# Performance work log

Hardware: AMD Instinct MI355X
Metric: run time of the kernel (lower is better)

## Reference

```python
import jax, jax.numpy as jnp
import numpy as np

B, S, E, H, NQ, FF = 2, 2048, 768, 12, 8, 3072
DK = E // H
EPS = 1e-5


def _layernorm(x, g, b):
    m = jnp.mean(x, axis=-1, keepdims=True)
    v = jnp.mean((x - m) ** 2, axis=-1, keepdims=True)
    return (x - m) * jax.lax.rsqrt(v + EPS) * g + b


def setup_inputs() -> dict:
    key = jax.random.key(0)
    ks = jax.random.split(key, 12)
    s = 0.02
    return {
        'x': jax.random.normal(ks[0], (B, S, E), dtype=jnp.float32),
        'W_o': jax.random.normal(ks[1], (E, E), dtype=jnp.float32) * s,
        'b_o': jnp.zeros((E,), dtype=jnp.float32),
        'g1': jnp.ones((E,), dtype=jnp.float32),
        'be1': jnp.zeros((E,), dtype=jnp.float32),
        'g2': jnp.ones((E,), dtype=jnp.float32),
        'be2': jnp.zeros((E,), dtype=jnp.float32),
        'ry': jax.random.normal(ks[2], (NQ,), dtype=jnp.float32),
        'W1': jax.random.normal(ks[3], (NQ, FF), dtype=jnp.float32) * s,
        'b1': jnp.zeros((FF,), dtype=jnp.float32),
        'W2': jax.random.normal(ks[4], (FF, E), dtype=jnp.float32) * s,
        'b2': jnp.zeros((E,), dtype=jnp.float32),
    }


def reference(x, W_o, b_o, g1, be1, g2, be2, ry, W1, b1, W2, b2):
    # --- multi-head self-attention (q = k = v = x, no QKV projection) ---
    q = x.reshape(B, S, H, DK).transpose(0, 2, 1, 3)  # [B,H,S,DK]
    scores = jnp.einsum('bhqd,bhkd->bhqk', q, q) / jnp.sqrt(jnp.float32(DK))
    attn = jax.nn.softmax(scores, axis=-1)
    out = jnp.einsum('bhqk,bhkd->bhqd', attn, q)
    out = out.transpose(0, 2, 1, 3).reshape(B, S, E)
    attn_out = out @ W_o + b_o

    x = _layernorm(x + attn_out, g1, be1)

    # --- quantum FFN: per-wire RX(x_i) encode, RY(ry_i), <Z> = cos(x_i)*cos(ry_i) ---
    q_meas = jnp.cos(x[..., :NQ]) * jnp.cos(ry)  # [B,S,NQ]
    ffn_out = jax.nn.relu(q_meas @ W1 + b1) @ W2 + b2

    return _layernorm(x + ffn_out, g2, be2)
```

## Files before the change

### kernel.cpp

```cpp
#include <hip/hip_runtime.h>
#include <hip/hip_bf16.h>

#define B_  2
#define S_  2048
#define E_  768
#define H_  12
#define DK_ 64
#define NQ_ 8
#define FF_ 3072
#define EPS_ 1e-5f

typedef __attribute__((ext_vector_type(8))) short short8;
typedef __attribute__((ext_vector_type(4))) float f32x4;
typedef __hip_bfloat16 bf16;

__device__ __forceinline__ bf16 f2bh(float f) { return __float2bfloat16(f); }
__device__ __forceinline__ short f2b(float f) {
    bf16 h = __float2bfloat16(f);
    return *reinterpret_cast<short*>(&h);
}

__device__ __forceinline__ int swz(int row, int col) {
    return (col & 7) | ((((col >> 3) ^ (row & 7)) & 7) << 3);
}

__device__ __forceinline__ f32x4 mfma16(short8 a, short8 b, f32x4 c) {
    return __builtin_amdgcn_mfma_f32_16x16x32_bf16(a, b, c, 0, 0, 0);
}

__device__ __forceinline__ void gload16(const bf16* g, bf16* l) {
    __builtin_amdgcn_global_load_lds(
        (__attribute__((address_space(1))) void*)g,
        (__attribute__((address_space(3))) void*)l, 16, 0, 0);
}

__global__ __launch_bounds__(256) void prep_xall(const float* __restrict__ x,
                                                 bf16* __restrict__ xb,
                                                 bf16* __restrict__ xT) {
    __shared__ float tile[32][33];
    int e0 = blockIdx.x * 32, s0 = blockIdx.y * 32;
    int tx = threadIdx.x & 31, ty = threadIdx.x >> 5;
    int b = s0 >> 11, sl0 = s0 & 2047;
#pragma unroll
    for (int i = 0; i < 4; i++) {
        int row = ty + i * 8;
        float v = x[(size_t)(s0 + row) * E_ + e0 + tx];
        tile[row][tx] = v;
        xb[(size_t)(s0 + row) * E_ + e0 + tx] = f2bh(v);
    }
    __syncthreads();
#pragma unroll
    for (int i = 0; i < 4; i++) {
        int row = ty + i * 8;
        xT[((size_t)b * E_ + e0 + row) * S_ + sl0 + tx] = f2bh(tile[tx][row]);
    }
}

__global__ __launch_bounds__(256) void prep_cvt(const float* __restrict__ x,
                                                bf16* __restrict__ xb, int n4) {
    int i = blockIdx.x * 256 + threadIdx.x;
    if (i >= n4) return;
    float4 f = *(const float4*)(x + (size_t)i * 4);
    short4 sv;
    sv.x = f2b(f.x); sv.y = f2b(f.y); sv.z = f2b(f.z); sv.w = f2b(f.w);
    *(short4*)((short*)xb + (size_t)i * 4) = sv;
}

__global__ __launch_bounds__(256) void transpose_cvt(const float* __restrict__ W,
                                                     bf16* __restrict__ WT,
                                                     int K, int N) {
    __shared__ float tile[32][33];
    int k0 = blockIdx.y * 32, n0 = blockIdx.x * 32;
    int tx = threadIdx.x & 31, ty = threadIdx.x >> 5;
#pragma unroll
    for (int i = 0; i < 4; i++) {
        int row = ty + i * 8;
        tile[row][tx] = W[(size_t)(k0 + row) * N + n0 + tx];
    }
    __syncthreads();
#pragma unroll
    for (int i = 0; i < 4; i++) {
        int row = ty + i * 8;
        WT[(size_t)(n0 + row) * K + k0 + tx] = f2bh(tile[tx][row]);
    }
}

__global__ __launch_bounds__(256) void prep_w1t(const float* __restrict__ W1,
                                                bf16* __restrict__ W1bT) {
    int k = blockIdx.x * 256 + threadIdx.x;
    if (k >= FF_) return;
    short8 v;
#pragma unroll
    for (int i = 0; i < NQ_; i++) v[i] = f2b(W1[(size_t)i * FF_ + k]);
    *(short8*)(W1bT + (size_t)k * NQ_) = v;
}

template<bool XT>
__global__ __launch_bounds__(256) void attn_kernel(const bf16* __restrict__ xb,
                                                   const bf16* __restrict__ xT,
                                                   bf16* __restrict__ out) {
    const int qtiles = S_ / 64;
    const int nwg = B_ * H_ * qtiles;
    int o = blockIdx.x;
    int blk = (o & 7) * (nwg >> 3) + (o >> 3);
    int qt = blk % qtiles;
    int hh = (blk / qtiles) % H_;
    int bb = blk / (qtiles * H_);
    const bf16* base = xb + (size_t)bb * S_ * E_ + hh * DK_;
    const bf16* baseT = xT + ((size_t)bb * E_ + hh * DK_) * S_;

    __shared__ __align__(16) bf16 Ks[2][64][64];
    __shared__ __align__(16) bf16 Vt[2][64][64];
    __shared__ __align__(16) bf16 Pl[4][16][64];

    int t = threadIdx.x;
    int w = t >> 6, l = t & 63, c = l & 15, g = l >> 4;

    short8 qf[2];
    {
        const bf16* qp = base + (size_t)(qt * 64 + w * 16 + c) * E_;
        qf[0] = *(const short8*)(qp + g * 8);
        qf[1] = *(const short8*)(qp + 32 + g * 8);
    }

    f32x4 oacc[4];
    float l_part[4];
#pragma unroll
    for (int n = 0; n < 4; n++) { oacc[n] = (f32x4){0.f, 0.f, 0.f, 0.f}; l_part[n] = 0.f; }

    int skey = t & 63;
    int scb0 = t >> 6;

    short8 preK[2], preV[2];
#pragma unroll
    for (int it = 0; it < 2; it++) {
        preK[it] = *(const short8*)(base + (size_t)skey * E_ + (scb0 + it * 4) * 8);
        if (XT)
            preV[it] = *(const short8*)(baseT + (size_t)skey * S_ + (scb0 + it * 4) * 8);
    }
#pragma unroll
    for (int it = 0; it < 2; it++) {
        int cb = scb0 + it * 4;
        *(short8*)&Ks[0][skey][swz(skey, cb * 8)] = preK[it];
        if (XT) {
            *(short8*)&Vt[0][skey][swz(skey, cb * 8)] = preV[it];
        } else {
#pragma unroll
            for (int j = 0; j < 8; j++) {
                int d = cb * 8 + j;
                short sv = preK[it][j];
                Vt[0][d][swz(d, skey)] = *reinterpret_cast<bf16*>(&sv);
            }
        }
    }
#pragma unroll
    for (int it = 0; it < 2; it++) {
        preK[it] = *(const short8*)(base + (size_t)(64 + skey) * E_ + (scb0 + it * 4) * 8);
        if (XT)
            preV[it] = *(const short8*)(baseT + (size_t)skey * S_ + 64 + (scb0 + it * 4) * 8);
    }
    __syncthreads();

    int cur = 0;
    for (int kt = 0; kt < S_ / 64; kt++, cur ^= 1) {
        int nxt = cur ^ 1;
        if (kt + 1 < S_ / 64) {
#pragma unroll
            for (int it = 0; it < 2; it++) {
                int cb = scb0 + it * 4;
                *(short8*)&Ks[nxt][skey][swz(skey, cb * 8)] = preK[it];
                if (XT) {
                    *(short8*)&Vt[nxt][skey][swz(skey, cb * 8)] = preV[it];
                } else {
#pragma unroll
                    for (int j = 0; j < 8; j++) {
                        int d = cb * 8 + j;
                        short sv = preK[it][j];
                        Vt[nxt][d][swz(d, skey)] = *reinterpret_cast<bf16*>(&sv);
                    }
                }
            }
        }
        if (kt + 2 < S_ / 64) {
#pragma unroll
            for (int it = 0; it < 2; it++) {
                preK[it] = *(const short8*)(base + (size_t)((kt + 2) * 64 + skey) * E_ + (scb0 + it * 4) * 8);
                if (XT)
                    preV[it] = *(const short8*)(baseT + (size_t)skey * S_ + (kt + 2) * 64 + (scb0 + it * 4) * 8);
            }
        }

        f32x4 sfr[4];
        __builtin_amdgcn_s_setprio(1);
#pragma unroll
        for (int n = 0; n < 4; n++) {
            sfr[n] = (f32x4){0.f, 0.f, 0.f, 0.f};
#pragma unroll
            for (int kh = 0; kh < 2; kh++) {
                const short8 bfr = *(const short8*)&Ks[cur][n * 16 + c][swz(n * 16 + c, kh * 32 + g * 8)];
                sfr[n] = mfma16(qf[kh], bfr, sfr[n]);
            }
        }
        __builtin_amdgcn_s_setprio(0);
#pragma unroll
        for (int jj = 0; jj < 4; jj++) {
            float pv[4];
#pragma unroll
            for (int n = 0; n < 4; n++)
                pv[n] = exp2f(sfr[n][jj] * 0.18033688f);
            l_part[jj] += (pv[0] + pv[1]) + (pv[2] + pv[3]);
            int r = g * 4 + jj;
#pragma unroll
            for (int n = 0; n < 4; n++)
                Pl[w][r][swz(r, n * 16 + c)] = f2bh(pv[n]);
        }

        __builtin_amdgcn_s_setprio(1);
#pragma unroll
        for (int ks = 0; ks < 2; ks++) {
            short8 vb[4];
#pragma unroll
            for (int dn = 0; dn < 4; dn++)
                vb[dn] = *(const short8*)&Vt[cur][dn * 16 + c][swz(dn * 16 + c, ks * 32 + g * 8)];
            const short8 pa = *(const short8*)&Pl[w][c][swz(c, ks * 32 + g * 8)];
#pragma unroll
            for (int dn = 0; dn < 4; dn++)
                oacc[dn] = mfma16(pa, vb[dn], oacc[dn]);
        }
        __builtin_amdgcn_s_setprio(0);
        __syncthreads();
    }

#pragma unroll
    for (int jj = 0; jj < 4; jj++) {
        float lv = l_part[jj];
#pragma unroll
        for (int msk = 1; msk < 16; msk <<= 1) lv += __shfl_xor(lv, msk);
        float inv = 1.f / lv;
        size_t ro = ((size_t)bb * S_ + qt * 64 + w * 16 + g * 4 + jj) * E_ + hh * DK_;
#pragma unroll
        for (int dn = 0; dn < 4; dn++)
            out[ro + dn * 16 + c] = f2bh(oacc[dn][jj] * inv);
    }
}

__global__ __launch_bounds__(256) void gemm_bf16(const bf16* __restrict__ A,
                                                 const bf16* __restrict__ BT,
                                                 const float* __restrict__ bias,
                                                 bf16* __restrict__ C,
                                                 int M, int N, int K) {
    __shared__ __align__(16) bf16 As2[2][64][64];
    __shared__ __align__(16) bf16 Bs2[2][64][64];
    int nbx = gridDim.x, nwg = nbx * gridDim.y;
    int id = blockIdx.y * nbx + blockIdx.x;
    int id2 = (nwg & 7) ? id : ((id & 7) * (nwg >> 3) + (id >> 3));
    int row0 = (id2 / nbx) * 64, col0 = (id2 % nbx) * 64;
    int t = threadIdx.x, w = t >> 6, l = t & 63, c = l & 15, g = l >> 4;

    f32x4 acc[4];
#pragma unroll
    for (int n = 0; n < 4; n++) acc[n] = (f32x4){0.f, 0.f, 0.f, 0.f};

    int srow = w * 16 + (l >> 3);
    int scol = ((l & 7) ^ ((l >> 3) & 7)) * 8;
    const bf16* apR0 = A + (size_t)(row0 + srow) * K + scol;
    const bf16* apR1 = A + (size_t)(row0 + srow + 8) * K + scol;
    const bf16* bpR0 = BT + (size_t)(col0 + srow) * K + scol;
    const bf16* bpR1 = BT + (size_t)(col0 + srow + 8) * K + scol;

    gload16(apR0, &As2[0][w * 16][0]);
    gload16(apR1, &As2[0][w * 16 + 8][0]);
    gload16(bpR0, &Bs2[0][w * 16][0]);
    gload16(bpR1, &Bs2[0][w * 16 + 8][0]);
    __syncthreads();

    int cur = 0;
    for (int k0 = 0; k0 < K; k0 += 64, cur ^= 1) {
        int nxt = cur ^ 1;
        if (k0 + 64 < K) {
            gload16(apR0 + k0 + 64, &As2[nxt][w * 16][0]);
            gload16(apR1 + k0 + 64, &As2[nxt][w * 16 + 8][0]);
            gload16(bpR0 + k0 + 64, &Bs2[nxt][w * 16][0]);
            gload16(bpR1 + k0 + 64, &Bs2[nxt][w * 16 + 8][0]);
        }
#pragma unroll
        for (int kh = 0; kh < 2; kh++) {
            const short8 af = *(const short8*)&As2[cur][w * 16 + c][swz(w * 16 + c, kh * 32 + g * 8)];
#pragma unroll
            for (int n = 0; n < 4; n++) {
                const short8 bfr = *(const short8*)&Bs2[cur][n * 16 + c][swz(n * 16 + c, kh * 32 + g * 8)];
                acc[n] = mfma16(af, bfr, acc[n]);
            }
        }
        __syncthreads();
    }
#pragma unroll
    for (int jj = 0; jj < 4; jj++) {
        int row = row0 + w * 16 + g * 4 + jj;
#pragma unroll
        for (int n = 0; n < 4; n++) {
            int col = col0 + n * 16 + c;
            C[(size_t)row * N + col] = f2bh(acc[n][jj] + bias[col]);
        }
    }
}

__global__ __launch_bounds__(256) void gemm2_mfma(const float* __restrict__ xln,
                                                  const float* __restrict__ ry,
                                                  const bf16* __restrict__ W1bT,
                                                  const float* __restrict__ b1,
                                                  const bf16* __restrict__ W2bT,
                                                  const float* __restrict__ b2,
                                                  bf16* __restrict__ C) {
    __shared__ __align__(16) bf16 As[64][64];
    __shared__ __align__(16) bf16 Bs[2][64][64];
    __shared__ __align__(16) bf16 W1t[2][64][8];
    __shared__ __align__(16) bf16 qm_s[64][8];
    const int nbx = E_ / 64;
    const int nwg = nbx * (B_ * S_ / 64);
    int id = blockIdx.y * nbx + blockIdx.x;
    int id2 = (id & 7) * (nwg >> 3) + (id >> 3);
    int row0 = (id2 / nbx) * 64, col0 = (id2 % nbx) * 64;
    int t = threadIdx.x, w = t >> 6, l = t & 63, c = l & 15, g = l >> 4;

    if (t < 64) {
        const float* xp = xln + (size_t)(row0 + t) * E_;
#pragma unroll
        for (int i = 0; i < NQ_; i++)
            qm_s[t][i] = f2bh(cosf(xp[i]) * cosf(ry[i]));
    }

    f32x4 acc[4];
#pragma unroll
    for (int n = 0; n < 4; n++) acc[n] = (f32x4){0.f, 0.f, 0.f, 0.f};

    int srow = w * 16 + (l >> 3);
    int scol = ((l & 7) ^ ((l >> 3) & 7)) * 8;
    const bf16* bpR0 = W2bT + (size_t)(col0 + srow) * FF_ + scol;
    const bf16* bpR1 = W2bT + (size_t)(col0 + srow + 8) * FF_ + scol;

    gload16(bpR0, &Bs[0][w * 16][0]);
    gload16(bpR1, &Bs[0][w * 16 + 8][0]);
    short8 preW;
    if (t < 64) {
        preW = *(const short8*)(W1bT + (size_t)t * NQ_);
        *(short8*)&W1t[0][t][0] = preW;
        preW = *(const short8*)(W1bT + (size_t)(64 + t) * NQ_);
    }
    __syncthreads();

    short8 zz = {0, 0, 0, 0, 0, 0, 0, 0};
    short8 aq = zz;
    if (g == 0) aq = *(const short8*)&qm_s[w * 16 + c][0];

    int cur = 0;
    for (int k0 = 0; k0 < FF_; k0 += 64, cur ^= 1) {
        float b1c[4];
#pragma unroll
        for (int n = 0; n < 4; n++) b1c[n] = b1[k0 + n * 16 + c];

        int nxt = cur ^ 1;
        if (k0 + 64 < FF_) {
            gload16(bpR0 + k0 + 64, &Bs[nxt][w * 16][0]);
            gload16(bpR1 + k0 + 64, &Bs[nxt][w * 16 + 8][0]);
            if (t < 64) *(short8*)&W1t[nxt][t][0] = preW;
        }
        if (k0 + 128 < FF_) {
            if (t < 64) preW = *(const short8*)(W1bT + (size_t)(k0 + 128 + t) * NQ_);
        }

        f32x4 zero4 = {0.f, 0.f, 0.f, 0.f};
#pragma unroll
        for (int n = 0; n < 4; n++) {
            short8 bw = zz;
            if (g == 0) bw = *(const short8*)&W1t[cur][n * 16 + c][0];
            f32x4 hfr = mfma16(aq, bw, zero4);
#pragma unroll
            for (int jj = 0; jj < 4; jj++) {
                float hv = fmaxf(hfr[jj] + b1c[n], 0.f);
                int r = w * 16 + g * 4 + jj;
                As[r][swz(r, n * 16 + c)] = f2bh(hv);
            }
        }

#pragma unroll
        for (int kh = 0; kh < 2; kh++) {
            const short8 af = *(const short8*)&As[w * 16 + c][swz(w * 16 + c, kh * 32 + g * 8)];
#pragma unroll
            for (int n = 0; n < 4; n++) {
                const short8 bfr = *(const short8*)&Bs[cur][n * 16 + c][swz(n * 16 + c, kh * 32 + g * 8)];
                acc[n] = mfma16(af, bfr, acc[n]);
            }
        }
        __syncthreads();
    }
#pragma unroll
    for (int jj = 0; jj < 4; jj++) {
        int row = row0 + w * 16 + g * 4 + jj;
#pragma unroll
        for (int n = 0; n < 4; n++) {
            int col = col0 + n * 16 + c;
            C[(size_t)row * E_ + col] = f2bh(acc[n][jj] + b2[col]);
        }
    }
}

__global__ __launch_bounds__(256) void gemm2_fused(const float* __restrict__ xln,
                                                   const float* __restrict__ ry,
                                                   const float* __restrict__ W1,
                                                   const float* __restrict__ b1,
                                                   const float* __restrict__ W2,
                                                   const float* __restrict__ b2,
                                                   bf16* __restrict__ C) {
    __shared__ __align__(16) bf16 As[64][64];
    __shared__ __align__(16) bf16 Bst[64][64];
    __shared__ float qmS[64][NQ_];
    int row0 = blockIdx.y * 64, col0 = blockIdx.x * 64;
    int t = threadIdx.x, w = t >> 6, l = t & 63, c = l & 15, g = l >> 4;

    for (int idx = t; idx < 64 * NQ_; idx += 256) {
        int r = idx >> 3, i = idx & 7;
        qmS[r][i] = cosf(xln[(size_t)(row0 + r) * E_ + i]) * cosf(ry[i]);
    }

    f32x4 acc[4];
#pragma unroll
    for (int n = 0; n < 4; n++) acc[n] = (f32x4){0.f, 0.f, 0.f, 0.f};

    int kl = t & 63, rg = (t >> 6) * 16;
    int brow = t >> 4, bcol = (t & 15) * 4;

    for (int k0 = 0; k0 < FF_; k0 += 64) {
        __syncthreads();
        {
            float w1v[NQ_];
#pragma unroll
            for (int i = 0; i < NQ_; i++) w1v[i] = W1[i * FF_ + k0 + kl];
            float b1v = b1[k0 + kl];
#pragma unroll
            for (int r16 = 0; r16 < 16; r16++) {
                int r = rg + r16;
                float sh = b1v;
#pragma unroll
                for (int i = 0; i < NQ_; i++) sh += qmS[r][i] * w1v[i];
                As[r][swz(r, kl)] = f2bh(fmaxf(sh, 0.f));
            }
        }
#pragma unroll
        for (int it = 0; it < 4; it++) {
            int kk = brow + it * 16;
            float4 v = *(const float4*)(W2 + (size_t)(k0 + kk) * E_ + col0 + bcol);
            Bst[bcol + 0][swz(bcol + 0, kk)] = f2bh(v.x);
            Bst[bcol + 1][swz(bcol + 1, kk)] = f2bh(v.y);
            Bst[bcol + 2][swz(bcol + 2, kk)] = f2bh(v.z);
            Bst[bcol + 3][swz(bcol + 3, kk)] = f2bh(v.w);
        }
        __syncthreads();
#pragma unroll
        for (int kh = 0; kh < 2; kh++) {
            const short8 af = *(const short8*)&As[w * 16 + c][swz(w * 16 + c, kh * 32 + g * 8)];
#pragma unroll
            for (int n = 0; n < 4; n++) {
                const short8 bfr = *(const short8*)&Bst[n * 16 + c][swz(n * 16 + c, kh * 32 + g * 8)];
                acc[n] = mfma16(af, bfr, acc[n]);
            }
        }
    }
#pragma unroll
    for (int jj = 0; jj < 4; jj++) {
        int row = row0 + w * 16 + g * 4 + jj;
#pragma unroll
        for (int n = 0; n < 4; n++) {
            int col = col0 + n * 16 + c;
            C[(size_t)row * E_ + col] = f2bh(acc[n][jj] + b2[col]);
        }
    }
}

__global__ __launch_bounds__(256) void ln_add_b(const float* __restrict__ X,
                                                const bf16* __restrict__ Yb,
                                                const float* __restrict__ g,
                                                const float* __restrict__ be,
                                                float* __restrict__ out) {
    int r = blockIdx.x;
    const size_t off = (size_t)r * E_;
    int t = threadIdx.x;
    float v[3];
    float s = 0.f, s2 = 0.f;
#pragma unroll
    for (int j = 0; j < 3; j++) {
        int e = t + j * 256;
        float val = X[off + e] + __bfloat162float(Yb[off + e]);
        v[j] = val; s += val; s2 += val * val;
    }
#pragma unroll
    for (int msk = 32; msk > 0; msk >>= 1) {
        s += __shfl_xor(s, msk);
        s2 += __shfl_xor(s2, msk);
    }
    __shared__ float red[8];
    int lane = t & 63, wv = t >> 6;
    if (lane == 0) { red[wv] = s; red[4 + wv] = s2; }
    __syncthreads();
    if (t == 0) {
        red[0] = red[0] + red[1] + red[2] + red[3];
        red[4] = red[4] + red[5] + red[6] + red[7];
    }
    __syncthreads();
    float mean = red[0] * (1.f / E_);
    float var = red[4] * (1.f / E_) - mean * mean;
    float inv = rsqrtf(var + EPS_);
#pragma unroll
    for (int j = 0; j < 3; j++) {
        int e = t + j * 256;
        out[off + e] = (v[j] - mean) * inv * g[e] + be[e];
    }
}

extern "C" void kernel_launch(void* const* d_in, const int* in_sizes, int n_in,
                              void* d_out, int out_size, void* d_ws, size_t ws_size,
                              hipStream_t stream) {
    const float* x   = (const float*)d_in[0];
    const float* W_o = (const float*)d_in[1];
    const float* b_o = (const float*)d_in[2];
    const float* g1  = (const float*)d_in[3];
    const float* be1 = (const float*)d_in[4];
    const float* g2  = (const float*)d_in[5];
    const float* be2 = (const float*)d_in[6];
    const float* ry  = (const float*)d_in[7];
    const float* W1  = (const float*)d_in[8];
    const float* b1  = (const float*)d_in[9];
    const float* W2  = (const float*)d_in[10];
    const float* b2  = (const float*)d_in[11];
    float* out = (float*)d_out;

    const size_t BSE = (size_t)B_ * S_ * E_;
    char* ws = (char*)d_ws;

    const size_t FAST_NEED = 43696128;
    bool fast = ws_size >= FAST_NEED;

    bf16* xb    = (bf16*)(ws + 0);
    bf16* attnb = (bf16*)(ws + 6291456);
    bf16* WobT  = fast ? (bf16*)(ws + 12582912) : (bf16*)(ws + 18874368);
    bf16* W2bT  = (bf16*)(ws + 13762560);
    bf16* tmp1b = fast ? (bf16*)(ws + 18481152) : (bf16*)(ws + 12582912);
    float* xln  = (float*)(ws + (fast ? 24772608 : 20054016));
    bf16* W1bT  = (bf16*)(ws + 37355520);
    bf16* xT    = (bf16*)(ws + 37404672);
    bf16* tmp2b = tmp1b;

    if (fast) {
        prep_xall<<<dim3(E_ / 32, B_ * S_ / 32), 256, 0, stream>>>(x, xb, xT);
        transpose_cvt<<<dim3(E_ / 32, FF_ / 32), 256, 0, stream>>>(W2, W2bT, FF_, E_);
        prep_w1t<<<dim3(FF_ / 256), 256, 0, stream>>>(W1, W1bT);
    } else {
        prep_cvt<<<dim3((int)((BSE / 4 + 255) / 256)), 256, 0, stream>>>(x, xb, (int)(BSE / 4));
    }
    transpose_cvt<<<dim3(E_ / 32, E_ / 32), 256, 0, stream>>>(W_o, WobT, E_, E_);

    if (fast)
        attn_kernel<true><<<dim3(B_ * H_ * (S_ / 64)), 256, 0, stream>>>(xb, xT, attnb);
    else
        attn_kernel<false><<<dim3(B_ * H_ * (S_ / 64)), 256, 0, stream>>>(xb, xb, attnb);

    gemm_bf16<<<dim3(E_ / 64, (B_ * S_) / 64), 256, 0, stream>>>(
        attnb, WobT, b_o, tmp1b, B_ * S_, E_, E_);
    ln_add_b<<<dim3(B_ * S_), 256, 0, stream>>>(x, tmp1b, g1, be1, xln);

    if (fast) {
        gemm2_mfma<<<dim3(E_ / 64, (B_ * S_) / 64), 256, 0, stream>>>(
            xln, ry, W1bT, b1, W2bT, b2, tmp2b);
    } else {
        gemm2_fused<<<dim3(E_ / 64, (B_ * S_) / 64), 256, 0, stream>>>(
            xln, ry, W1, b1, W2, b2, tmp2b);
    }
    ln_add_b<<<dim3(B_ * S_), 256, 0, stream>>>(xln, tmp2b, g2, be2, out);
}
```

Baseline: 164.3 us.

## Use direct-to-LDS loads, transposed MFMA operands and prescaled Q in attention

The attention kernel's transposed-input path now streams K and V tiles straight into LDS with global_load_lds, replacing the register prefetch and LDS store. Operands to the QK MFMA are swapped so each lane holds four consecutive keys of one query row, which allows packed 8-byte stores of P and a single running row sum. The softmax scale is folded into Q at load time, which removes a multiply per score but adds an extra bf16 rounding. The fused FFN kernel applies the same operand swap to pack its hidden-activation stores and loads the bias as vectors.

```diff
diff --git a/kernel.cpp b/kernel.cpp
--- a/kernel.cpp
+++ b/kernel.cpp
@@ -11,6 +11,7 @@
 #define EPS_ 1e-5f
 
 typedef __attribute__((ext_vector_type(8))) short short8;
+typedef __attribute__((ext_vector_type(4))) short shortv4;
 typedef __attribute__((ext_vector_type(4))) float f32x4;
 typedef __hip_bfloat16 bf16;
 
@@ -18,6 +19,10 @@
 __device__ __forceinline__ short f2b(float f) {
     bf16 h = __float2bfloat16(f);
     return *reinterpret_cast<short*>(&h);
+}
+__device__ __forceinline__ float b2f(short s) {
+    bf16 h = *reinterpret_cast<bf16*>(&s);
+    return __bfloat162float(h);
 }
 
 __device__ __forceinline__ int swz(int row, int col) {
@@ -101,6 +106,7 @@
                                                    bf16* __restrict__ out) {
     const int qtiles = S_ / 64;
     const int nwg = B_ * H_ * qtiles;
+    const int NT = S_ / 64;
     int o = blockIdx.x;
     int blk = (o & 7) * (nwg >> 3) + (o >> 3);
     int qt = blk % qtiles;
@@ -119,32 +125,41 @@
     short8 qf[2];
     {
         const bf16* qp = base + (size_t)(qt * 64 + w * 16 + c) * E_;
-        qf[0] = *(const short8*)(qp + g * 8);
-        qf[1] = *(const short8*)(qp + 32 + g * 8);
+#pragma unroll
+        for (int kh = 0; kh < 2; kh++) {
+            short8 v = *(const short8*)(qp + kh * 32 + g * 8);
+#pragma unroll
+            for (int j = 0; j < 8; j++) v[j] = f2b(b2f(v[j]) * 0.18033688f);
+            qf[kh] = v;
+        }
     }
 
     f32x4 oacc[4];
-    float l_part[4];
-#pragma unroll
-    for (int n = 0; n < 4; n++) { oacc[n] = (f32x4){0.f, 0.f, 0.f, 0.f}; l_part[n] = 0.f; }
-
-    int skey = t & 63;
-    int scb0 = t >> 6;
-
-    short8 preK[2], preV[2];
-#pragma unroll
-    for (int it = 0; it < 2; it++) {
-        preK[it] = *(const short8*)(base + (size_t)skey * E_ + (scb0 + it * 4) * 8);
-        if (XT)
-            preV[it] = *(const short8*)(baseT + (size_t)skey * S_ + (scb0 + it * 4) * 8);
-    }
-#pragma unroll
-    for (int it = 0; it < 2; it++) {
-        int cb = scb0 + it * 4;
-        *(short8*)&Ks[0][skey][swz(skey, cb * 8)] = preK[it];
-        if (XT) {
-            *(short8*)&Vt[0][skey][swz(skey, cb * 8)] = preV[it];
-        } else {
+    float lsum = 0.f;
+#pragma unroll
+    for (int n = 0; n < 4; n++) oacc[n] = (f32x4){0.f, 0.f, 0.f, 0.f};
+
+    int rr = l >> 3;
+    int scol = ((l & 7) ^ (rr & 7)) * 8;
+    const bf16* srcK = base + (size_t)(w * 16 + rr) * E_ + scol;
+    const bf16* srcV = baseT + (size_t)(w * 16 + rr) * S_ + scol;
+
+    int skey = t & 63, scb0 = t >> 6;
+    short8 preK[2];
+
+    if (XT) {
+        gload16(srcK, &Ks[0][w * 16][0]);
+        gload16(srcK + 8 * E_, &Ks[0][w * 16 + 8][0]);
+        gload16(srcV, &Vt[0][w * 16][0]);
+        gload16(srcV + 8 * S_, &Vt[0][w * 16 + 8][0]);
+    } else {
+#pragma unroll
+        for (int it = 0; it < 2; it++)
+            preK[it] = *(const short8*)(base + (size_t)skey * E_ + (scb0 + it * 4) * 8);
+#pragma unroll
+        for (int it = 0; it < 2; it++) {
+            int cb = scb0 + it * 4;
+            *(short8*)&Ks[0][skey][swz(skey, cb * 8)] = preK[it];
 #pragma unroll
             for (int j = 0; j < 8; j++) {
                 int d = cb * 8 + j;
@@ -152,26 +167,28 @@
                 Vt[0][d][swz(d, skey)] = *reinterpret_cast<bf16*>(&sv);
             }
         }
-    }
-#pragma unroll
-    for (int it = 0; it < 2; it++) {
-        preK[it] = *(const short8*)(base + (size_t)(64 + skey) * E_ + (scb0 + it * 4) * 8);
-        if (XT)
-            preV[it] = *(const short8*)(baseT + (size_t)skey * S_ + 64 + (scb0 + it * 4) * 8);
+#pragma unroll
+        for (int it = 0; it < 2; it++)
+            preK[it] = *(const short8*)(base + (size_t)(64 + skey) * E_ + (scb0 + it * 4) * 8);
     }
     __syncthreads();
 
     int cur = 0;
-    for (int kt = 0; kt < S_ / 64; kt++, cur ^= 1) {
+    for (int kt = 0; kt < NT; kt++, cur ^= 1) {
         int nxt = cur ^ 1;
-        if (kt + 1 < S_ / 64) {
-#pragma unroll
-            for (int it = 0; it < 2; it++) {
-                int cb = scb0 + it * 4;
-                *(short8*)&Ks[nxt][skey][swz(skey, cb * 8)] = preK[it];
-                if (XT) {
-                    *(short8*)&Vt[nxt][skey][swz(skey, cb * 8)] = preV[it];
-                } else {
+        if (kt + 1 < NT) {
+            if (XT) {
+                const bf16* sK = srcK + (size_t)(kt + 1) * 64 * E_;
+                const bf16* sV = srcV + (kt + 1) * 64;
+                gload16(sK, &Ks[nxt][w * 16][0]);
+                gload16(sK + 8 * E_, &Ks[nxt][w * 16 + 8][0]);
+                gload16(sV, &Vt[nxt][w * 16][0]);
+                gload16(sV + 8 * S_, &Vt[nxt][w * 16 + 8][0]);
+            } else {
+#pragma unroll
+                for (int it = 0; it < 2; it++) {
+                    int cb = scb0 + it * 4;
+                    *(short8*)&Ks[nxt][skey][swz(skey, cb * 8)] = preK[it];
 #pragma unroll
                     for (int j = 0; j < 8; j++) {
                         int d = cb * 8 + j;
@@ -181,13 +198,10 @@
                 }
             }
         }
-        if (kt + 2 < S_ / 64) {
-#pragma unroll
-            for (int it = 0; it < 2; it++) {
+        if (!XT && kt + 2 < NT) {
+#pragma unroll
+            for (int it = 0; it < 2; it++)
                 preK[it] = *(const short8*)(base + (size_t)((kt + 2) * 64 + skey) * E_ + (scb0 + it * 4) * 8);
-                if (XT)
-                    preV[it] = *(const short8*)(baseT + (size_t)skey * S_ + (kt + 2) * 64 + (scb0 + it * 4) * 8);
-            }
         }
 
         f32x4 sfr[4];
@@ -198,21 +212,21 @@
 #pragma unroll
             for (int kh = 0; kh < 2; kh++) {
                 const short8 bfr = *(const short8*)&Ks[cur][n * 16 + c][swz(n * 16 + c, kh * 32 + g * 8)];
-                sfr[n] = mfma16(qf[kh], bfr, sfr[n]);
+                sfr[n] = mfma16(bfr, qf[kh], sfr[n]);
             }
         }
         __builtin_amdgcn_s_setprio(0);
-#pragma unroll
-        for (int jj = 0; jj < 4; jj++) {
+
+#pragma unroll
+        for (int n = 0; n < 4; n++) {
             float pv[4];
 #pragma unroll
-            for (int n = 0; n < 4; n++)
-                pv[n] = exp2f(sfr[n][jj] * 0.18033688f);
-            l_part[jj] += (pv[0] + pv[1]) + (pv[2] + pv[3]);
-            int r = g * 4 + jj;
-#pragma unroll
-            for (int n = 0; n < 4; n++)
-                Pl[w][r][swz(r, n * 16 + c)] = f2bh(pv[n]);
+            for (int jj = 0; jj < 4; jj++) pv[jj] = exp2f(sfr[n][jj]);
+            lsum += (pv[0] + pv[1]) + (pv[2] + pv[3]);
+            shortv4 pk;
+#pragma unroll
+            for (int jj = 0; jj < 4; jj++) pk[jj] = f2b(pv[jj]);
+            *(shortv4*)&Pl[w][c][swz(c, n * 16 + g * 4)] = pk;
         }
 
         __builtin_amdgcn_s_setprio(1);
@@ -232,11 +246,10 @@
     }
 
 #pragma unroll
+    for (int msk = 16; msk < 64; msk <<= 1) lsum += __shfl_xor(lsum, msk);
+#pragma unroll
     for (int jj = 0; jj < 4; jj++) {
-        float lv = l_part[jj];
-#pragma unroll
-        for (int msk = 1; msk < 16; msk <<= 1) lv += __shfl_xor(lv, msk);
-        float inv = 1.f / lv;
+        float inv = 1.f / __shfl(lsum, g * 4 + jj);
         size_t ro = ((size_t)bb * S_ + qt * 64 + w * 16 + g * 4 + jj) * E_ + hh * DK_;
 #pragma unroll
         for (int dn = 0; dn < 4; dn++)
@@ -355,9 +368,10 @@
 
     int cur = 0;
     for (int k0 = 0; k0 < FF_; k0 += 64, cur ^= 1) {
-        float b1c[4];
-#pragma unroll
-        for (int n = 0; n < 4; n++) b1c[n] = b1[k0 + n * 16 + c];
+        f32x4 b1v[4];
+#pragma unroll
+        for (int n = 0; n < 4; n++)
+            b1v[n] = *(const f32x4*)(b1 + k0 + n * 16 + g * 4);
 
         int nxt = cur ^ 1;
         if (k0 + 64 < FF_) {
@@ -370,17 +384,17 @@
         }
 
         f32x4 zero4 = {0.f, 0.f, 0.f, 0.f};
+        int r = w * 16 + c;
 #pragma unroll
         for (int n = 0; n < 4; n++) {
             short8 bw = zz;
             if (g == 0) bw = *(const short8*)&W1t[cur][n * 16 + c][0];
-            f32x4 hfr = mfma16(aq, bw, zero4);
-#pragma unroll
-            for (int jj = 0; jj < 4; jj++) {
-                float hv = fmaxf(hfr[jj] + b1c[n], 0.f);
-                int r = w * 16 + g * 4 + jj;
-                As[r][swz(r, n * 16 + c)] = f2bh(hv);
-            }
+            f32x4 hfr = mfma16(bw, aq, zero4);
+            shortv4 pk;
+#pragma unroll
+            for (int jj = 0; jj < 4; jj++)
+                pk[jj] = f2b(fmaxf(hfr[jj] + b1v[n][jj], 0.f));
+            *(shortv4*)&As[r][swz(r, n * 16 + g * 4)] = pk;
         }
 
 #pragma unroll
```

Result: faster. 149.3 us (-9.1%).
